# Optimization experiments

Hardware: AMD Instinct MI355X
Metric: run time of the kernel (lower is better)

The kernel has to match this reference:

```python
import math
import jax, jax.numpy as jnp
import numpy as np

NUM_HEADS = 16
EPS = 1e-6


def _rotate_half(t):
    t1, t2 = jnp.split(t, 2, axis=-1)
    return jnp.concatenate([-t2, t1], axis=-1)


def _rmsnorm(t, w):
    # compute in fp32 like the torch module, then cast back and apply affine
    x32 = t.astype(jnp.float32)
    r = jax.lax.rsqrt(jnp.mean(x32 * x32, axis=-1, keepdims=True) + EPS)
    return (x32 * r).astype(t.dtype) * w


def setup_inputs() -> dict:
    key = jax.random.key(0)
    ks = jax.random.split(key, 12)
    B, N, C, T = 8, 1024, 1024, 1024
    hd2 = (C // NUM_HEADS) // 2  # 32
    inp = {
        "x": jax.random.normal(ks[0], (B, N, C), jnp.float32),
        "temb": jax.random.normal(ks[1], (B, T), jnp.float32),
        "cos_y": jax.random.uniform(ks[2], (1, 1, N, hd2), jnp.float32, -1.0, 1.0),
        "sin_y": jax.random.uniform(ks[3], (1, 1, N, hd2), jnp.float32, -1.0, 1.0),
        "cos_x": jax.random.uniform(ks[4], (1, 1, N, hd2), jnp.float32, -1.0, 1.0),
        "sin_x": jax.random.uniform(ks[5], (1, 1, N, hd2), jnp.float32, -1.0, 1.0),
        # params; weights stored (in, out) so y = x @ W + b (== torch x @ W.T)
        "Wqkv": jax.random.normal(ks[6], (C, 3 * C), jnp.float32) * 0.02,
        "bqkv": jnp.zeros((3 * C,), jnp.float32),
        "Wt": jax.random.normal(ks[7], (T, 3 * C), jnp.float32) * 0.02,
        "bt": jnp.zeros((3 * C,), jnp.float32),
        "Wp": jax.random.normal(ks[8], (C, C), jnp.float32) * 0.02,
        "bp": jnp.zeros((C,), jnp.float32),
        "qn_w": jnp.ones((C // NUM_HEADS,), jnp.float32),
        "kn_w": jnp.ones((C // NUM_HEADS,), jnp.float32),
    }
    return inp


def reference(x, temb, cos_y, sin_y, cos_x, sin_x,
              Wqkv, bqkv, Wt, bt, Wp, bp, qn_w, kn_w):
    B, N, C = x.shape
    H = NUM_HEADS
    hd = C // H
    # fused QKV projection + additive time conditioning
    qkv = x @ Wqkv + bqkv + (temb @ Wt + bt)[:, None, :]         # [B,N,3C]
    qkv = qkv.reshape(B, N, 3, H, hd).transpose(2, 0, 3, 1, 4)    # [3,B,H,N,hd]
    q, k, v = qkv[0], qkv[1], qkv[2]
    # per-head QK RMSNorm with affine
    q = _rmsnorm(q, qn_w)
    k = _rmsnorm(k, kn_w)
    # axial 2D RoPE on the y-half and x-half of head_dim
    qy, qx = jnp.split(q, 2, axis=-1)
    ky, kx = jnp.split(k, 2, axis=-1)
    qy = qy * cos_y + _rotate_half(qy) * sin_y
    ky = ky * cos_y + _rotate_half(ky) * sin_y
    qx = qx * cos_x + _rotate_half(qx) * sin_x
    kx = kx * cos_x + _rotate_half(kx) * sin_x
    q = jnp.concatenate([qy, qx], axis=-1)
    k = jnp.concatenate([ky, kx], axis=-1)
    # scaled dot-product attention (no dropout at eval)
    scale = 1.0 / math.sqrt(hd)
    scores = jnp.einsum('bhqd,bhkd->bhqk', q, k) * scale
    attn = jax.nn.softmax(scores, axis=-1)
    out = jnp.einsum('bhqk,bhkd->bhqd', attn, v)                  # [B,H,N,hd]
    out = out.transpose(0, 2, 1, 3).reshape(B, N, C)
    return out @ Wp + bp
```

## Files before the change

### kernel.cpp

```cpp
#include <hip/hip_runtime.h>
#include <cstdint>

typedef unsigned short u16;
typedef __bf16 bf16x8 __attribute__((ext_vector_type(8)));
typedef float f32x4 __attribute__((ext_vector_type(4)));

__device__ __forceinline__ u16 f2bf(float f) {
  __bf16 h = (__bf16)f;
  return __builtin_bit_cast(u16, h);
}
__device__ __forceinline__ float bf2f(u16 u) {
  union { uint32_t u; float f; } v; v.u = ((uint32_t)u) << 16;
  return v.f;
}

__device__ __forceinline__ void gload16(const void* g, const void* l) {
  __builtin_amdgcn_global_load_lds(
      (const __attribute__((address_space(1))) uint32_t*)(uintptr_t)g,
      (__attribute__((address_space(3))) uint32_t*)(uintptr_t)l, 16, 0, 0);
}

__device__ __forceinline__ f32x4 mfma16(bf16x8 a, bf16x8 b, f32x4 c) {
  return __builtin_amdgcn_mfma_f32_16x16x32_bf16(a, b, c, 0, 0, 0);
}

__device__ __forceinline__ int swz(int row, int col) {
  return row * 64 + ((((col >> 3) ^ (row & 7)) << 3) | (col & 7));
}

__global__ __launch_bounds__(256)
void k_cvt(const float* __restrict__ src, u16* __restrict__ dst, int n4) {
  int i = blockIdx.x * 256 + threadIdx.x;
  if (i >= n4) return;
  float4 v = ((const float4*)src)[i];
  union { u16 s[4]; uint2 u; } o;
  o.s[0] = f2bf(v.x); o.s[1] = f2bf(v.y); o.s[2] = f2bf(v.z); o.s[3] = f2bf(v.w);
  ((uint2*)dst)[i] = o.u;
}

__global__ __launch_bounds__(256)
void k_transpose(const float* __restrict__ src, u16* __restrict__ dst, int R, int Cc) {
  __shared__ u16 t[64 * 66];
  int r0 = blockIdx.y * 64, c0 = blockIdx.x * 64;
  #pragma unroll
  for (int i = 0; i < 16; i++) {
    int e = i * 256 + threadIdx.x;
    int rl = e >> 6, cl = e & 63;
    t[cl * 66 + rl] = f2bf(src[(size_t)(r0 + rl) * Cc + c0 + cl]);
  }
  __syncthreads();
  #pragma unroll
  for (int i = 0; i < 16; i++) {
    int e = i * 256 + threadIdx.x;
    int ro = e >> 6, co = e & 63;
    dst[(size_t)(c0 + ro) * R + r0 + co] = t[ro * 66 + co];
  }
}

__global__ __launch_bounds__(256)
void k_temb_part(const float* __restrict__ temb, const float* __restrict__ Wt,
                 float* __restrict__ part) {
  const int j = blockIdx.x * 256 + threadIdx.x;
  const int k0 = blockIdx.y * 32;
  float acc[8];
  #pragma unroll
  for (int b = 0; b < 8; b++) acc[b] = 0.f;
  #pragma unroll 4
  for (int k = k0; k < k0 + 32; k++) {
    float wv = Wt[(size_t)k * 3072 + j];
    #pragma unroll
    for (int b = 0; b < 8; b++) acc[b] += temb[b * 1024 + k] * wv;
  }
  float* p = part + (size_t)blockIdx.y * 24576 + j;
  #pragma unroll
  for (int b = 0; b < 8; b++) p[b * 3072] = acc[b];
}

__global__ __launch_bounds__(256)
void k_temb_red(const float* __restrict__ part, const float* __restrict__ bt,
                const float* __restrict__ bqkv, float* __restrict__ tcomb) {
  const int j = blockIdx.x * 256 + threadIdx.x;
  const int b = blockIdx.y;
  const float* p = part + b * 3072 + j;
  float a = bt[j] + bqkv[j];
  #pragma unroll
  for (int kt = 0; kt < 32; kt++) a += p[(size_t)kt * 24576];
  tcomb[b * 3072 + j] = a;
}

template <int MODE>
__global__ __launch_bounds__(256, 2)
void k_gemm(const u16* __restrict__ A, const u16* __restrict__ Bt,
            u16* __restrict__ outb, float* __restrict__ outf,
            const float* __restrict__ bias, int K, int Ntot) {
  __shared__ u16 As[2][8192];
  __shared__ u16 Bs[2][4096];
  const int m0 = blockIdx.y * 256;
  const int n0 = blockIdx.x * 128;
  const int lane = threadIdx.x & 63;
  const int w = threadIdx.x >> 6;
  const int l15 = lane & 15;
  const int fo = (((lane >> 4) ^ ((lane >> 1) & 3)) << 3);
  const int srow = lane >> 2;
  const int schunk = (((lane & 3) ^ ((lane >> 3) & 3)) << 3);

  f32x4 acc[4][8];
  #pragma unroll
  for (int i = 0; i < 4; i++)
    #pragma unroll
    for (int j = 0; j < 8; j++) acc[i][j] = (f32x4){0.f, 0.f, 0.f, 0.f};

  const u16* Ag = A + (size_t)(m0 + srow) * K + schunk;
  const u16* Bg = Bt + (size_t)(n0 + srow) * K + schunk;

  const int iters = K >> 5;
  #pragma unroll
  for (int tt = 0; tt < 4; tt++) {
    int t = w * 4 + tt;
    gload16(Ag + (size_t)(16 * t) * K, &As[0][t * 512]);
  }
  #pragma unroll
  for (int tt = 0; tt < 2; tt++) {
    int t = w * 2 + tt;
    gload16(Bg + (size_t)(16 * t) * K, &Bs[0][t * 512]);
  }

  for (int it = 0; it < iters; it++) {
    __syncthreads();
    const int cur = it & 1;
    if (it + 1 < iters) {
      const int nxt = cur ^ 1;
      const int k1 = (it + 1) << 5;
      #pragma unroll
      for (int tt = 0; tt < 4; tt++) {
        int t = w * 4 + tt;
        gload16(Ag + (size_t)(16 * t) * K + k1, &As[nxt][t * 512]);
      }
      #pragma unroll
      for (int tt = 0; tt < 2; tt++) {
        int t = w * 2 + tt;
        gload16(Bg + (size_t)(16 * t) * K + k1, &Bs[nxt][t * 512]);
      }
    }
    bf16x8 af[4], bfr[8];
    #pragma unroll
    for (int i = 0; i < 4; i++)
      af[i] = *(const bf16x8*)&As[cur][(w * 64 + 16 * i + l15) * 32 + fo];
    #pragma unroll
    for (int j = 0; j < 8; j++)
      bfr[j] = *(const bf16x8*)&Bs[cur][(16 * j + l15) * 32 + fo];
    #pragma unroll
    for (int i = 0; i < 4; i++)
      #pragma unroll
      for (int j = 0; j < 8; j++)
        acc[i][j] = mfma16(af[i], bfr[j], acc[i][j]);
  }

  const int rl = (lane >> 4) * 4;
  #pragma unroll
  for (int i = 0; i < 4; i++) {
    #pragma unroll
    for (int j = 0; j < 8; j++) {
      #pragma unroll
      for (int r = 0; r < 4; r++) {
        int grow = m0 + w * 64 + 16 * i + rl + r;
        int gcol = n0 + 16 * j + l15;
        float v = acc[i][j][r];
        if (MODE == 0) {
          int b = grow >> 10;
          v += bias[b * Ntot + gcol];
          outb[(size_t)grow * Ntot + gcol] = f2bf(v);
        } else {
          v += bias[gcol];
          outf[(size_t)grow * Ntot + gcol] = v;
        }
      }
    }
  }
}

__global__ __launch_bounds__(256)
void k_rrv(const u16* __restrict__ qkv,
           const float* __restrict__ cos_y, const float* __restrict__ sin_y,
           const float* __restrict__ cos_x, const float* __restrict__ sin_x,
           const float* __restrict__ qn_w, const float* __restrict__ kn_w,
           u16* __restrict__ Qo, u16* __restrict__ Ko, u16* __restrict__ VT) {
  __shared__ u16 t[64 * 68];
  const int n0 = blockIdx.x * 64, h = blockIdx.y, b = blockIdx.z;
  const int bh = b * 16 + h;
  const int lane = threadIdx.x & 63, w = threadIdx.x >> 6;
  const int l15 = lane & 15, lg = lane >> 4;
  float4 qw = *(const float4*)(qn_w + l15 * 4);
  float4 kw = *(const float4*)(kn_w + l15 * 4);
  const float sgn = (lane & 4) ? 1.0f : -1.0f;
  const float* ct = (lane & 8) ? cos_x : cos_y;
  const float* st = (lane & 8) ? sin_x : sin_y;
  const float QSCALE = 0.18033688011112042f;

  #pragma unroll
  for (int rr = 0; rr < 4; rr++) {
    int row = n0 + w * 16 + rr * 4 + lg;
    size_t src = (size_t)(b * 1024 + row) * 3072 + h * 64 + l15 * 4;
    uint2 qu = *(const uint2*)(qkv + src);
    uint2 ku = *(const uint2*)(qkv + src + 1024);
    float q[4], k[4];
    q[0] = bf2f((u16)qu.x); q[1] = bf2f((u16)(qu.x >> 16));
    q[2] = bf2f((u16)qu.y); q[3] = bf2f((u16)(qu.y >> 16));
    k[0] = bf2f((u16)ku.x); k[1] = bf2f((u16)(ku.x >> 16));
    k[2] = bf2f((u16)ku.y); k[3] = bf2f((u16)(ku.y >> 16));
    float sq = q[0]*q[0] + q[1]*q[1] + q[2]*q[2] + q[3]*q[3];
    float sk = k[0]*k[0] + k[1]*k[1] + k[2]*k[2] + k[3]*k[3];
    #pragma unroll
    for (int m = 1; m < 16; m <<= 1) {
      sq += __shfl_xor(sq, m);
      sk += __shfl_xor(sk, m);
    }
    float rq = rsqrtf(sq * (1.0f / 64.0f) + 1e-6f);
    float rk = rsqrtf(sk * (1.0f / 64.0f) + 1e-6f);
    float4 cc = *(const float4*)(ct + (size_t)row * 32 + (lane & 7) * 4);
    float4 ss = *(const float4*)(st + (size_t)row * 32 + (lane & 7) * 4);
    float qn[4], kn[4];
    qn[0] = q[0]*rq*qw.x; qn[1] = q[1]*rq*qw.y; qn[2] = q[2]*rq*qw.z; qn[3] = q[3]*rq*qw.w;
    kn[0] = k[0]*rk*kw.x; kn[1] = k[1]*rk*kw.y; kn[2] = k[2]*rk*kw.z; kn[3] = k[3]*rk*kw.w;
    float c[4] = {cc.x, cc.y, cc.z, cc.w};
    float s[4] = {ss.x, ss.y, ss.z, ss.w};
    union { u16 e[4]; uint2 u; } oq, ok;
    #pragma unroll
    for (int j = 0; j < 4; j++) {
      float qp = __shfl_xor(qn[j], 4);
      float kp = __shfl_xor(kn[j], 4);
      oq.e[j] = f2bf((qn[j] * c[j] + sgn * qp * s[j]) * QSCALE);
      ok.e[j] = f2bf(kn[j] * c[j] + sgn * kp * s[j]);
    }
    size_t dst = ((size_t)bh * 1024 + row) * 64 + l15 * 4;
    *(uint2*)(Qo + dst) = oq.u;
    *(uint2*)(Ko + dst) = ok.u;
  }

  #pragma unroll
  for (int i = 0; i < 4; i++) {
    int e = i * 256 + threadIdx.x;
    int n = e >> 4, dc = e & 15;
    uint2 v = *(const uint2*)(qkv + (size_t)(b * 1024 + n0 + n) * 3072 + 2048 + h * 64 + dc * 4);
    t[(dc * 4 + 0) * 68 + n] = (u16)v.x;
    t[(dc * 4 + 1) * 68 + n] = (u16)(v.x >> 16);
    t[(dc * 4 + 2) * 68 + n] = (u16)v.y;
    t[(dc * 4 + 3) * 68 + n] = (u16)(v.y >> 16);
  }
  __syncthreads();
  #pragma unroll
  for (int i = 0; i < 4; i++) {
    int e = i * 256 + threadIdx.x;
    int d = e >> 4, nc = e & 15;
    const u16* p = &t[d * 68 + nc * 4];
    uint2 o;
    o.x = (uint32_t)p[0] | ((uint32_t)p[1] << 16);
    o.y = (uint32_t)p[2] | ((uint32_t)p[3] << 16);
    *(uint2*)(VT + ((size_t)bh * 64 + d) * 1024 + n0 + nc * 4) = o;
  }
}

__global__ __launch_bounds__(256, 2)
void k_attn(const u16* __restrict__ Q, const u16* __restrict__ Kb,
            const u16* __restrict__ VT, u16* __restrict__ Ob) {
  __shared__ u16 Ks[2][4096], VTs[2][4096], Ps[4][2048];
  const int lane = threadIdx.x & 63;
  const int w = threadIdx.x >> 6;
  const int bh = blockIdx.x;
  const int qt = blockIdx.y;
  const int b = bh >> 4, h = bh & 15;
  const size_t base = (size_t)bh * 65536;
  const int q0 = qt * 128;
  const int scol = ((lane & 7) ^ (lane >> 3)) * 8;
  const int lr = lane >> 3;

  bf16x8 aq[2][2];
  #pragma unroll
  for (int i = 0; i < 2; i++)
    #pragma unroll
    for (int s = 0; s < 2; s++)
      aq[i][s] = *(const bf16x8*)(Q + base +
          (size_t)(q0 + w * 32 + i * 16 + (lane & 15)) * 64 + s * 32 + (lane >> 4) * 8);

  f32x4 acc_o[2][4];
  float lpar[2][4];
  #pragma unroll
  for (int i = 0; i < 2; i++)
    #pragma unroll
    for (int r = 0; r < 4; r++) {
      acc_o[i][r] = (f32x4){0.f, 0.f, 0.f, 0.f};
      lpar[i][r] = 0.f;
    }

  #pragma unroll
  for (int tt = 0; tt < 2; tt++) {
    int t = w * 2 + tt;
    gload16(Kb + base + (size_t)(8 * t + lr) * 64 + scol, &Ks[0][t * 512]);
    gload16(VT + base + (size_t)(8 * t + lr) * 1024 + scol, &VTs[0][t * 512]);
  }

  for (int it = 0; it < 16; it++) {
    __syncthreads();
    const int cur = it & 1;
    if (it < 15) {
      const int nxt = cur ^ 1;
      const int j1 = (it + 1) * 64;
      #pragma unroll
      for (int tt = 0; tt < 2; tt++) {
        int t = w * 2 + tt;
        gload16(Kb + base + (size_t)(j1 + 8 * t + lr) * 64 + scol, &Ks[nxt][t * 512]);
        gload16(VT + base + (size_t)(8 * t + lr) * 1024 + j1 + scol, &VTs[nxt][t * 512]);
      }
    }
    const u16* K_ = Ks[cur];
    const u16* V_ = VTs[cur];

    f32x4 accs[2][4];
    #pragma unroll
    for (int i = 0; i < 2; i++)
      #pragma unroll
      for (int nt = 0; nt < 4; nt++) accs[i][nt] = (f32x4){0.f, 0.f, 0.f, 0.f};
    #pragma unroll
    for (int s = 0; s < 2; s++) {
      bf16x8 bk[4];
      #pragma unroll
      for (int nt = 0; nt < 4; nt++)
        bk[nt] = *(const bf16x8*)&K_[swz(nt * 16 + (lane & 15), s * 32 + (lane >> 4) * 8)];
      #pragma unroll
      for (int i = 0; i < 2; i++)
        #pragma unroll
        for (int nt = 0; nt < 4; nt++)
          accs[i][nt] = mfma16(aq[i][s], bk[nt], accs[i][nt]);
    }

    #pragma unroll
    for (int i = 0; i < 2; i++) {
      #pragma unroll
      for (int nt = 0; nt < 4; nt++) {
        #pragma unroll
        for (int r = 0; r < 4; r++) {
          float p = __builtin_amdgcn_exp2f(accs[i][nt][r]);
          lpar[i][r] += p;
          Ps[w][swz(i * 16 + (lane >> 4) * 4 + r, nt * 16 + (lane & 15))] = f2bf(p);
        }
      }
    }
    asm volatile("s_waitcnt lgkmcnt(0)" ::: "memory");

    #pragma unroll
    for (int s = 0; s < 2; s++) {
      bf16x8 bv[4];
      #pragma unroll
      for (int dt = 0; dt < 4; dt++)
        bv[dt] = *(const bf16x8*)&V_[swz(dt * 16 + (lane & 15), s * 32 + (lane >> 4) * 8)];
      #pragma unroll
      for (int i = 0; i < 2; i++) {
        bf16x8 ap = *(const bf16x8*)&Ps[w][swz(i * 16 + (lane & 15), s * 32 + (lane >> 4) * 8)];
        #pragma unroll
        for (int dt = 0; dt < 4; dt++)
          acc_o[i][dt] = mfma16(ap, bv[dt], acc_o[i][dt]);
      }
    }
  }

  #pragma unroll
  for (int i = 0; i < 2; i++) {
    float inv[4];
    #pragma unroll
    for (int r = 0; r < 4; r++) {
      float l = lpar[i][r];
      #pragma unroll
      for (int m = 1; m < 16; m <<= 1) l += __shfl_xor(l, m);
      inv[r] = 1.0f / l;
    }
    #pragma unroll
    for (int dt = 0; dt < 4; dt++)
      #pragma unroll
      for (int r = 0; r < 4; r++) {
        int row = q0 + w * 32 + i * 16 + (lane >> 4) * 4 + r;
        int col = h * 64 + dt * 16 + (lane & 15);
        Ob[((size_t)b * 1024 + row) * 1024 + col] = f2bf(acc_o[i][dt][r] * inv[r]);
      }
  }
}

extern "C" void kernel_launch(void* const* d_in, const int* in_sizes, int n_in,
                              void* d_out, int out_size, void* d_ws, size_t ws_size,
                              hipStream_t stream) {
  const float* x     = (const float*)d_in[0];
  const float* temb  = (const float*)d_in[1];
  const float* cos_y = (const float*)d_in[2];
  const float* sin_y = (const float*)d_in[3];
  const float* cos_x = (const float*)d_in[4];
  const float* sin_x = (const float*)d_in[5];
  const float* Wqkv  = (const float*)d_in[6];
  const float* bqkv  = (const float*)d_in[7];
  const float* Wt    = (const float*)d_in[8];
  const float* bt    = (const float*)d_in[9];
  const float* Wp    = (const float*)d_in[10];
  const float* bp    = (const float*)d_in[11];
  const float* qn_w  = (const float*)d_in[12];
  const float* kn_w  = (const float*)d_in[13];
  float* out = (float*)d_out;

  char* ws = (char*)d_ws;
  u16*   x_bf  = (u16*)(ws);
  u16*   WqkvT = (u16*)(ws + 16777216);
  u16*   WpT   = (u16*)(ws + 23068672);
  float* tcomb = (float*)(ws + 25165824);
  u16*   qkv   = (u16*)(ws + 25264128);
  u16*   Qb    = (u16*)(ws + 75595776);
  u16*   Kb    = (u16*)(ws + 92372992);
  u16*   VTb   = (u16*)(ws + 109150208);
  float* tpart = (float*)(ws + 125927424);
  u16*   att   = x_bf;

  k_cvt<<<8192, 256, 0, stream>>>(x, x_bf, 8192 * 1024 / 4);
  k_transpose<<<dim3(48, 16), 256, 0, stream>>>(Wqkv, WqkvT, 1024, 3072);
  k_transpose<<<dim3(16, 16), 256, 0, stream>>>(Wp, WpT, 1024, 1024);
  k_temb_part<<<dim3(12, 32), 256, 0, stream>>>(temb, Wt, tpart);
  k_temb_red<<<dim3(12, 8), 256, 0, stream>>>(tpart, bt, bqkv, tcomb);
  k_gemm<0><<<dim3(24, 32), 256, 0, stream>>>(x_bf, WqkvT, qkv, nullptr, tcomb, 1024, 3072);
  k_rrv<<<dim3(16, 16, 8), 256, 0, stream>>>(qkv, cos_y, sin_y, cos_x, sin_x,
                                             qn_w, kn_w, Qb, Kb, VTb);
  k_attn<<<dim3(128, 8), 256, 0, stream>>>(Qb, Kb, VTb, att);
  k_gemm<1><<<dim3(8, 32), 256, 0, stream>>>(att, WpT, nullptr, out, bp, 1024, 1024);
}
```

Before: 300.3 us.

## Restructure GEMM with 3-stage LDS pipeline, 128x256 tiles and XCD-aware block mapping

Rewrites the bf16 GEMM kernel used for the QKV and output projections. It moves to 512 threads with a 128x256 tile and BK=64, and triple-buffers the LDS tiles using explicit vmcnt waits so global loads run two stages ahead. It also remaps the 1D block id so consecutive tiles spread across the XCDs, and raises wave priority around the MFMA burst. The triple buffers take about 144KB of LDS, which limits occupancy to one block per CU and relies on a swizzle helper for conflict-free fragment reads.

```diff
diff --git a/kernel.cpp b/kernel.cpp
--- a/kernel.cpp
+++ b/kernel.cpp
@@ -89,83 +89,93 @@
 }
 
 template <int MODE>
-__global__ __launch_bounds__(256, 2)
+__global__ __launch_bounds__(512, 2)
 void k_gemm(const u16* __restrict__ A, const u16* __restrict__ Bt,
             u16* __restrict__ outb, float* __restrict__ outf,
             const float* __restrict__ bias, int K, int Ntot) {
-  __shared__ u16 As[2][8192];
-  __shared__ u16 Bs[2][4096];
-  const int m0 = blockIdx.y * 256;
-  const int n0 = blockIdx.x * 128;
+  __shared__ __align__(16) u16 As[3][128 * 64];
+  __shared__ __align__(16) u16 Bs[3][256 * 64];
+
+  const int nb = (int)gridDim.x;
+  const int chunk = nb >> 3;
+  const int bid = (int)blockIdx.x;
+  const int sb = (bid & 7) * chunk + (bid >> 3);
+  const int NBN = Ntot >> 8;
+  const int m0 = (sb / NBN) * 128;
+  const int n0 = (sb % NBN) * 256;
+
   const int lane = threadIdx.x & 63;
   const int w = threadIdx.x >> 6;
+  const int wm = w >> 2;
+  const int wn = w & 3;
   const int l15 = lane & 15;
-  const int fo = (((lane >> 4) ^ ((lane >> 1) & 3)) << 3);
-  const int srow = lane >> 2;
-  const int schunk = (((lane & 3) ^ ((lane >> 3) & 3)) << 3);
-
-  f32x4 acc[4][8];
+  const int g8 = (lane >> 4) * 8;
+
+  const int srow = lane >> 3;
+  const int schunk = ((lane & 7) ^ srow) * 8;
+  const u16* Ag = A + (size_t)(m0 + w * 16 + srow) * K + schunk;
+  const u16* Bg = Bt + (size_t)(n0 + w * 32 + srow) * K + schunk;
+
+  f32x4 acc[4][4];
   #pragma unroll
   for (int i = 0; i < 4; i++)
     #pragma unroll
-    for (int j = 0; j < 8; j++) acc[i][j] = (f32x4){0.f, 0.f, 0.f, 0.f};
-
-  const u16* Ag = A + (size_t)(m0 + srow) * K + schunk;
-  const u16* Bg = Bt + (size_t)(n0 + srow) * K + schunk;
-
-  const int iters = K >> 5;
-  #pragma unroll
-  for (int tt = 0; tt < 4; tt++) {
-    int t = w * 4 + tt;
-    gload16(Ag + (size_t)(16 * t) * K, &As[0][t * 512]);
-  }
-  #pragma unroll
-  for (int tt = 0; tt < 2; tt++) {
-    int t = w * 2 + tt;
-    gload16(Bg + (size_t)(16 * t) * K, &Bs[0][t * 512]);
-  }
-
-  for (int it = 0; it < iters; it++) {
-    __syncthreads();
-    const int cur = it & 1;
-    if (it + 1 < iters) {
-      const int nxt = cur ^ 1;
-      const int k1 = (it + 1) << 5;
-      #pragma unroll
-      for (int tt = 0; tt < 4; tt++) {
-        int t = w * 4 + tt;
-        gload16(Ag + (size_t)(16 * t) * K + k1, &As[nxt][t * 512]);
-      }
-      #pragma unroll
-      for (int tt = 0; tt < 2; tt++) {
-        int t = w * 2 + tt;
-        gload16(Bg + (size_t)(16 * t) * K + k1, &Bs[nxt][t * 512]);
-      }
-    }
-    bf16x8 af[4], bfr[8];
-    #pragma unroll
-    for (int i = 0; i < 4; i++)
-      af[i] = *(const bf16x8*)&As[cur][(w * 64 + 16 * i + l15) * 32 + fo];
-    #pragma unroll
-    for (int j = 0; j < 8; j++)
-      bfr[j] = *(const bf16x8*)&Bs[cur][(16 * j + l15) * 32 + fo];
-    #pragma unroll
-    for (int i = 0; i < 4; i++)
-      #pragma unroll
-      for (int j = 0; j < 8; j++)
-        acc[i][j] = mfma16(af[i], bfr[j], acc[i][j]);
+    for (int j = 0; j < 4; j++) acc[i][j] = (f32x4){0.f, 0.f, 0.f, 0.f};
+
+  auto stage = [&](int kt_, int buf_) {
+    const int ko = kt_ << 6;
+    #pragma unroll
+    for (int tt = 0; tt < 2; tt++)
+      gload16(Ag + (size_t)(tt * 8) * K + ko, &As[buf_][(w * 2 + tt) * 512]);
+    #pragma unroll
+    for (int tt = 0; tt < 4; tt++)
+      gload16(Bg + (size_t)(tt * 8) * K + ko, &Bs[buf_][(w * 4 + tt) * 512]);
+  };
+
+  const int NT = K >> 6;
+  stage(0, 0);
+  stage(1, 1);
+
+  int cur = 0;
+  for (int kt = 0; kt < NT; kt++) {
+    if (kt + 1 < NT) asm volatile("s_waitcnt vmcnt(6)" ::: "memory");
+    else             asm volatile("s_waitcnt vmcnt(0)" ::: "memory");
+    __builtin_amdgcn_s_barrier();
+    __builtin_amdgcn_sched_barrier(0);
+    if (kt + 2 < NT) stage(kt + 2, cur + 2 >= 3 ? cur - 1 : cur + 2);
+
+    bf16x8 af[2][4], bfr[2][4];
+    #pragma unroll
+    for (int s = 0; s < 2; s++) {
+      #pragma unroll
+      for (int mf = 0; mf < 4; mf++)
+        af[s][mf] = *(const bf16x8*)&As[cur][swz(wm * 64 + mf * 16 + l15, s * 32 + g8)];
+      #pragma unroll
+      for (int nf = 0; nf < 4; nf++)
+        bfr[s][nf] = *(const bf16x8*)&Bs[cur][swz(wn * 64 + nf * 16 + l15, s * 32 + g8)];
+    }
+    __builtin_amdgcn_s_setprio(1);
+    #pragma unroll
+    for (int mf = 0; mf < 4; mf++)
+      #pragma unroll
+      for (int nf = 0; nf < 4; nf++) {
+        acc[mf][nf] = mfma16(af[0][mf], bfr[0][nf], acc[mf][nf]);
+        acc[mf][nf] = mfma16(af[1][mf], bfr[1][nf], acc[mf][nf]);
+      }
+    __builtin_amdgcn_s_setprio(0);
+    cur = cur + 1 >= 3 ? 0 : cur + 1;
   }
 
   const int rl = (lane >> 4) * 4;
   #pragma unroll
-  for (int i = 0; i < 4; i++) {
-    #pragma unroll
-    for (int j = 0; j < 8; j++) {
+  for (int mf = 0; mf < 4; mf++) {
+    #pragma unroll
+    for (int nf = 0; nf < 4; nf++) {
       #pragma unroll
       for (int r = 0; r < 4; r++) {
-        int grow = m0 + w * 64 + 16 * i + rl + r;
-        int gcol = n0 + 16 * j + l15;
-        float v = acc[i][j][r];
+        int grow = m0 + wm * 64 + mf * 16 + rl + r;
+        int gcol = n0 + wn * 64 + nf * 16 + l15;
+        float v = acc[mf][nf][r];
         if (MODE == 0) {
           int b = grow >> 10;
           v += bias[b * Ntot + gcol];
@@ -420,9 +430,9 @@
   k_transpose<<<dim3(16, 16), 256, 0, stream>>>(Wp, WpT, 1024, 1024);
   k_temb_part<<<dim3(12, 32), 256, 0, stream>>>(temb, Wt, tpart);
   k_temb_red<<<dim3(12, 8), 256, 0, stream>>>(tpart, bt, bqkv, tcomb);
-  k_gemm<0><<<dim3(24, 32), 256, 0, stream>>>(x_bf, WqkvT, qkv, nullptr, tcomb, 1024, 3072);
+  k_gemm<0><<<dim3(768), 512, 0, stream>>>(x_bf, WqkvT, qkv, nullptr, tcomb, 1024, 3072);
   k_rrv<<<dim3(16, 16, 8), 256, 0, stream>>>(qkv, cos_y, sin_y, cos_x, sin_x,
                                              qn_w, kn_w, Qb, Kb, VTb);
   k_attn<<<dim3(128, 8), 256, 0, stream>>>(Qb, Kb, VTb, att);
-  k_gemm<1><<<dim3(8, 32), 256, 0, stream>>>(att, WpT, nullptr, out, bp, 1024, 1024);
-}
+  k_gemm<1><<<dim3(256), 512, 0, stream>>>(att, WpT, nullptr, out, bp, 1024, 1024);
+}
```

Measured after the change: 299.4 us. No clear change (-0.3%).

## Fuse QK RMSNorm, RoPE and V transpose into QKV GEMM epilogue

Applied to the files above, without the earlier changes.

The QKV GEMM epilogue now applies bias, per-head RMSNorm, axial RoPE and the Q scale directly from accumulators, writing Q/K in head-major layout. V tiles are transposed through shared memory and written as VT. This removes the separate k_rrv kernel and the bf16 qkv round-trip through global memory. In exchange the epilogue does more shuffles and rope-table loads, and its Q/K stores are 2-byte scattered writes.

```diff
diff --git a/kernel.cpp b/kernel.cpp
--- a/kernel.cpp
+++ b/kernel.cpp
@@ -91,10 +91,15 @@
 template <int MODE>
 __global__ __launch_bounds__(256, 2)
 void k_gemm(const u16* __restrict__ A, const u16* __restrict__ Bt,
-            u16* __restrict__ outb, float* __restrict__ outf,
-            const float* __restrict__ bias, int K, int Ntot) {
-  __shared__ u16 As[2][8192];
-  __shared__ u16 Bs[2][4096];
+            float* __restrict__ outf, const float* __restrict__ bias,
+            int K, int Ntot,
+            const float* __restrict__ cos_y, const float* __restrict__ sin_y,
+            const float* __restrict__ cos_x, const float* __restrict__ sin_x,
+            const float* __restrict__ qn_w, const float* __restrict__ kn_w,
+            u16* __restrict__ Qo, u16* __restrict__ Ko, u16* __restrict__ VTo) {
+  __shared__ u16 SM[24576];
+  u16* As = SM;
+  u16* Bs = SM + 16384;
   const int m0 = blockIdx.y * 256;
   const int n0 = blockIdx.x * 128;
   const int lane = threadIdx.x & 63;
@@ -117,12 +122,12 @@
   #pragma unroll
   for (int tt = 0; tt < 4; tt++) {
     int t = w * 4 + tt;
-    gload16(Ag + (size_t)(16 * t) * K, &As[0][t * 512]);
+    gload16(Ag + (size_t)(16 * t) * K, &As[t * 512]);
   }
   #pragma unroll
   for (int tt = 0; tt < 2; tt++) {
     int t = w * 2 + tt;
-    gload16(Bg + (size_t)(16 * t) * K, &Bs[0][t * 512]);
+    gload16(Bg + (size_t)(16 * t) * K, &Bs[t * 512]);
   }
 
   for (int it = 0; it < iters; it++) {
@@ -134,21 +139,21 @@
       #pragma unroll
       for (int tt = 0; tt < 4; tt++) {
         int t = w * 4 + tt;
-        gload16(Ag + (size_t)(16 * t) * K + k1, &As[nxt][t * 512]);
+        gload16(Ag + (size_t)(16 * t) * K + k1, &As[nxt * 8192 + t * 512]);
       }
       #pragma unroll
       for (int tt = 0; tt < 2; tt++) {
         int t = w * 2 + tt;
-        gload16(Bg + (size_t)(16 * t) * K + k1, &Bs[nxt][t * 512]);
+        gload16(Bg + (size_t)(16 * t) * K + k1, &Bs[nxt * 4096 + t * 512]);
       }
     }
     bf16x8 af[4], bfr[8];
     #pragma unroll
     for (int i = 0; i < 4; i++)
-      af[i] = *(const bf16x8*)&As[cur][(w * 64 + 16 * i + l15) * 32 + fo];
+      af[i] = *(const bf16x8*)&As[cur * 8192 + (w * 64 + 16 * i + l15) * 32 + fo];
     #pragma unroll
     for (int j = 0; j < 8; j++)
-      bfr[j] = *(const bf16x8*)&Bs[cur][(16 * j + l15) * 32 + fo];
+      bfr[j] = *(const bf16x8*)&Bs[cur * 4096 + (16 * j + l15) * 32 + fo];
     #pragma unroll
     for (int i = 0; i < 4; i++)
       #pragma unroll
@@ -157,106 +162,102 @@
   }
 
   const int rl = (lane >> 4) * 4;
-  #pragma unroll
-  for (int i = 0; i < 4; i++) {
-    #pragma unroll
-    for (int j = 0; j < 8; j++) {
+
+  if (MODE == 1) {
+    #pragma unroll
+    for (int i = 0; i < 4; i++)
+      #pragma unroll
+      for (int j = 0; j < 8; j++)
+        #pragma unroll
+        for (int r = 0; r < 4; r++) {
+          int grow = m0 + w * 64 + 16 * i + rl + r;
+          int gcol = n0 + 16 * j + l15;
+          outf[(size_t)grow * Ntot + gcol] = acc[i][j][r] + bias[gcol];
+        }
+    return;
+  }
+
+  const int bidx = m0 >> 10;
+  float tc[8];
+  #pragma unroll
+  for (int j = 0; j < 8; j++) tc[j] = bias[bidx * 3072 + n0 + 16 * j + l15];
+
+  if (n0 < 2048) {
+    const bool isQ = (n0 < 1024);
+    u16* dst = isQ ? Qo : Ko;
+    const float* nw = isQ ? qn_w : kn_w;
+    const float osc = isQ ? 0.18033688011112042f : 1.0f;
+    const int hbase = (n0 & 1023) >> 6;
+    float wv[8];
+    #pragma unroll
+    for (int j = 0; j < 8; j++) wv[j] = nw[(16 * j + l15) & 63];
+
+    #pragma unroll
+    for (int i = 0; i < 4; i++) {
       #pragma unroll
       for (int r = 0; r < 4; r++) {
         int grow = m0 + w * 64 + 16 * i + rl + r;
-        int gcol = n0 + 16 * j + l15;
-        float v = acc[i][j][r];
-        if (MODE == 0) {
-          int b = grow >> 10;
-          v += bias[b * Ntot + gcol];
-          outb[(size_t)grow * Ntot + gcol] = f2bf(v);
-        } else {
-          v += bias[gcol];
-          outf[(size_t)grow * Ntot + gcol] = v;
+        int n = grow & 1023;
+        float v[8];
+        #pragma unroll
+        for (int j = 0; j < 8; j++) v[j] = acc[i][j][r] + tc[j];
+        float sA = v[0]*v[0] + v[1]*v[1] + v[2]*v[2] + v[3]*v[3];
+        float sB = v[4]*v[4] + v[5]*v[5] + v[6]*v[6] + v[7]*v[7];
+        #pragma unroll
+        for (int m = 1; m < 16; m <<= 1) {
+          sA += __shfl_xor(sA, m);
+          sB += __shfl_xor(sB, m);
         }
-      }
-    }
-  }
-}
-
-__global__ __launch_bounds__(256)
-void k_rrv(const u16* __restrict__ qkv,
-           const float* __restrict__ cos_y, const float* __restrict__ sin_y,
-           const float* __restrict__ cos_x, const float* __restrict__ sin_x,
-           const float* __restrict__ qn_w, const float* __restrict__ kn_w,
-           u16* __restrict__ Qo, u16* __restrict__ Ko, u16* __restrict__ VT) {
-  __shared__ u16 t[64 * 68];
-  const int n0 = blockIdx.x * 64, h = blockIdx.y, b = blockIdx.z;
-  const int bh = b * 16 + h;
-  const int lane = threadIdx.x & 63, w = threadIdx.x >> 6;
-  const int l15 = lane & 15, lg = lane >> 4;
-  float4 qw = *(const float4*)(qn_w + l15 * 4);
-  float4 kw = *(const float4*)(kn_w + l15 * 4);
-  const float sgn = (lane & 4) ? 1.0f : -1.0f;
-  const float* ct = (lane & 8) ? cos_x : cos_y;
-  const float* st = (lane & 8) ? sin_x : sin_y;
-  const float QSCALE = 0.18033688011112042f;
-
-  #pragma unroll
-  for (int rr = 0; rr < 4; rr++) {
-    int row = n0 + w * 16 + rr * 4 + lg;
-    size_t src = (size_t)(b * 1024 + row) * 3072 + h * 64 + l15 * 4;
-    uint2 qu = *(const uint2*)(qkv + src);
-    uint2 ku = *(const uint2*)(qkv + src + 1024);
-    float q[4], k[4];
-    q[0] = bf2f((u16)qu.x); q[1] = bf2f((u16)(qu.x >> 16));
-    q[2] = bf2f((u16)qu.y); q[3] = bf2f((u16)(qu.y >> 16));
-    k[0] = bf2f((u16)ku.x); k[1] = bf2f((u16)(ku.x >> 16));
-    k[2] = bf2f((u16)ku.y); k[3] = bf2f((u16)(ku.y >> 16));
-    float sq = q[0]*q[0] + q[1]*q[1] + q[2]*q[2] + q[3]*q[3];
-    float sk = k[0]*k[0] + k[1]*k[1] + k[2]*k[2] + k[3]*k[3];
-    #pragma unroll
-    for (int m = 1; m < 16; m <<= 1) {
-      sq += __shfl_xor(sq, m);
-      sk += __shfl_xor(sk, m);
-    }
-    float rq = rsqrtf(sq * (1.0f / 64.0f) + 1e-6f);
-    float rk = rsqrtf(sk * (1.0f / 64.0f) + 1e-6f);
-    float4 cc = *(const float4*)(ct + (size_t)row * 32 + (lane & 7) * 4);
-    float4 ss = *(const float4*)(st + (size_t)row * 32 + (lane & 7) * 4);
-    float qn[4], kn[4];
-    qn[0] = q[0]*rq*qw.x; qn[1] = q[1]*rq*qw.y; qn[2] = q[2]*rq*qw.z; qn[3] = q[3]*rq*qw.w;
-    kn[0] = k[0]*rk*kw.x; kn[1] = k[1]*rk*kw.y; kn[2] = k[2]*rk*kw.z; kn[3] = k[3]*rk*kw.w;
-    float c[4] = {cc.x, cc.y, cc.z, cc.w};
-    float s[4] = {ss.x, ss.y, ss.z, ss.w};
-    union { u16 e[4]; uint2 u; } oq, ok;
-    #pragma unroll
-    for (int j = 0; j < 4; j++) {
-      float qp = __shfl_xor(qn[j], 4);
-      float kp = __shfl_xor(kn[j], 4);
-      oq.e[j] = f2bf((qn[j] * c[j] + sgn * qp * s[j]) * QSCALE);
-      ok.e[j] = f2bf(kn[j] * c[j] + sgn * kp * s[j]);
-    }
-    size_t dst = ((size_t)bh * 1024 + row) * 64 + l15 * 4;
-    *(uint2*)(Qo + dst) = oq.u;
-    *(uint2*)(Ko + dst) = ok.u;
-  }
-
-  #pragma unroll
-  for (int i = 0; i < 4; i++) {
-    int e = i * 256 + threadIdx.x;
-    int n = e >> 4, dc = e & 15;
-    uint2 v = *(const uint2*)(qkv + (size_t)(b * 1024 + n0 + n) * 3072 + 2048 + h * 64 + dc * 4);
-    t[(dc * 4 + 0) * 68 + n] = (u16)v.x;
-    t[(dc * 4 + 1) * 68 + n] = (u16)(v.x >> 16);
-    t[(dc * 4 + 2) * 68 + n] = (u16)v.y;
-    t[(dc * 4 + 3) * 68 + n] = (u16)(v.y >> 16);
-  }
-  __syncthreads();
-  #pragma unroll
-  for (int i = 0; i < 4; i++) {
-    int e = i * 256 + threadIdx.x;
-    int d = e >> 4, nc = e & 15;
-    const u16* p = &t[d * 68 + nc * 4];
-    uint2 o;
-    o.x = (uint32_t)p[0] | ((uint32_t)p[1] << 16);
-    o.y = (uint32_t)p[2] | ((uint32_t)p[3] << 16);
-    *(uint2*)(VT + ((size_t)bh * 64 + d) * 1024 + n0 + nc * 4) = o;
+        float rA = rsqrtf(sA * (1.0f / 64.0f) + 1e-6f);
+        float rB = rsqrtf(sB * (1.0f / 64.0f) + 1e-6f);
+        float u[8];
+        #pragma unroll
+        for (int j = 0; j < 8; j++) u[j] = v[j] * (j < 4 ? rA : rB) * wv[j];
+        const float* cy = cos_y + (size_t)n * 32;
+        const float* sy = sin_y + (size_t)n * 32;
+        const float* cx = cos_x + (size_t)n * 32;
+        const float* sx = sin_x + (size_t)n * 32;
+        #pragma unroll
+        for (int j = 0; j < 8; j++) {
+          int dh = ((j & 1) << 4) + l15;
+          float c = (j & 2) ? cx[dh] : cy[dh];
+          float s = (j & 2) ? sx[dh] : sy[dh];
+          float sgn = (j & 1) ? 1.0f : -1.0f;
+          float o = (u[j] * c + sgn * u[j ^ 1] * s) * osc;
+          int h = hbase + (j >> 2);
+          int d = (16 * j + l15) & 63;
+          dst[((size_t)(bidx * 16 + h) * 1024 + n) * 64 + d] = f2bf(o);
+        }
+      }
+    }
+  } else {
+    __syncthreads();
+    u16* T = SM;
+    const int vbase = bidx * 1024 + (n0 & 1023);
+    const int nb0 = m0 & 1023;
+    #pragma unroll
+    for (int p = 0; p < 2; p++) {
+      if ((w >> 1) == p) {
+        #pragma unroll
+        for (int i = 0; i < 4; i++)
+          #pragma unroll
+          for (int j = 0; j < 8; j++)
+            #pragma unroll
+            for (int r = 0; r < 4; r++) {
+              int nl = (w & 1) * 64 + 16 * i + rl + r;
+              T[(16 * j + l15) * 136 + nl] = f2bf(acc[i][j][r] + tc[j]);
+            }
+      }
+      __syncthreads();
+      #pragma unroll
+      for (int itr = 0; itr < 8; itr++) {
+        int e = itr * 256 + threadIdx.x;
+        int row = e >> 4, ch = e & 15;
+        uint4 val = *(const uint4*)&T[row * 136 + ch * 8];
+        *(uint4*)(VTo + ((size_t)(vbase + row)) * 1024 + nb0 + p * 128 + ch * 8) = val;
+      }
+      __syncthreads();
+    }
   }
 }
 
@@ -408,7 +409,6 @@
   u16*   WqkvT = (u16*)(ws + 16777216);
   u16*   WpT   = (u16*)(ws + 23068672);
   float* tcomb = (float*)(ws + 25165824);
-  u16*   qkv   = (u16*)(ws + 25264128);
   u16*   Qb    = (u16*)(ws + 75595776);
   u16*   Kb    = (u16*)(ws + 92372992);
   u16*   VTb   = (u16*)(ws + 109150208);
@@ -420,9 +420,12 @@
   k_transpose<<<dim3(16, 16), 256, 0, stream>>>(Wp, WpT, 1024, 1024);
   k_temb_part<<<dim3(12, 32), 256, 0, stream>>>(temb, Wt, tpart);
   k_temb_red<<<dim3(12, 8), 256, 0, stream>>>(tpart, bt, bqkv, tcomb);
-  k_gemm<0><<<dim3(24, 32), 256, 0, stream>>>(x_bf, WqkvT, qkv, nullptr, tcomb, 1024, 3072);
-  k_rrv<<<dim3(16, 16, 8), 256, 0, stream>>>(qkv, cos_y, sin_y, cos_x, sin_x,
-                                             qn_w, kn_w, Qb, Kb, VTb);
+  k_gemm<0><<<dim3(24, 32), 256, 0, stream>>>(
+      x_bf, WqkvT, nullptr, tcomb, 1024, 3072,
+      cos_y, sin_y, cos_x, sin_x, qn_w, kn_w, Qb, Kb, VTb);
   k_attn<<<dim3(128, 8), 256, 0, stream>>>(Qb, Kb, VTb, att);
-  k_gemm<1><<<dim3(8, 32), 256, 0, stream>>>(att, WpT, nullptr, out, bp, 1024, 1024);
-}
+  k_gemm<1><<<dim3(8, 32), 256, 0, stream>>>(
+      att, WpT, out, bp, 1024, 1024,
+      nullptr, nullptr, nullptr, nullptr, nullptr, nullptr,
+      nullptr, nullptr, nullptr);
+}
```

Result: slower. 306.8 us (+2.1%).
